# Performance work log

Hardware: AMD Instinct MI355X
Metric: run time of the kernel (lower is better)

The kernel has to match this reference:

```python
import jax, jax.numpy as jnp
import numpy as np

N_EXPERTS = 8
N_SHARED = 1
N_ROUTED = N_EXPERTS - N_SHARED          # 7
TOP_K_ROUTED = 3 - N_SHARED              # 2 routed experts per token
C = 1024
H = 4 * C


def _mlp(x, w_fc, w_proj):
    # x: [n, C]; w_fc: [C, H]; w_proj: [H, C]; exact (erf) GELU like torch nn.GELU
    return jax.nn.gelu(x @ w_fc, approximate=False) @ w_proj


def setup_inputs() -> dict:
    key = jax.random.key(0)
    ks = jax.random.split(key, 6)
    s = 0.02
    return {
        "x": jax.random.normal(ks[0], (4, 2048, C), dtype=jnp.float32),
        "gate_w": jax.random.normal(ks[1], (N_ROUTED, C), dtype=jnp.float32) * s,
        "lb_bias": jnp.zeros((N_ROUTED,), dtype=jnp.float32),
        "shared_wfc": jax.random.normal(ks[2], (C, H), dtype=jnp.float32) * s,
        "shared_wproj": jax.random.normal(ks[3], (H, C), dtype=jnp.float32) * s,
        "routed_wfc": jax.random.normal(ks[4], (N_ROUTED, C, H), dtype=jnp.float32) * s,
        "routed_wproj": jax.random.normal(ks[5], (N_ROUTED, H, C), dtype=jnp.float32) * s,
    }


def reference(x, gate_w, lb_bias, shared_wfc, shared_wproj, routed_wfc, routed_wproj):
    B, T, Cc = x.shape
    xt = x.reshape(-1, Cc)                       # [n, C]
    n = xt.shape[0]

    # shared expert(s) applied to every token
    shared_out = _mlp(xt, shared_wfc, shared_wproj)

    # routing
    routed_logits = xt @ gate_w.T                # [n, E_r]
    sel_logits = routed_logits + lb_bias
    _, topk_idx = jax.lax.top_k(sel_logits, TOP_K_ROUTED)   # [n, k]
    routed_probs = jax.nn.softmax(routed_logits.astype(jnp.float32), axis=-1)
    topk_w = jnp.take_along_axis(routed_probs, topk_idx, axis=-1)  # [n, k]

    # per-token combine weights over routed experts: [n, E_r]
    cw = jnp.zeros((n, N_ROUTED), dtype=jnp.float32)
    cw = cw.at[jnp.arange(n)[:, None], topk_idx].add(topk_w)

    # dispatch-combine: small fixed loop over routed experts
    routed_out = jnp.zeros_like(xt)
    for e in range(N_ROUTED):
        y = _mlp(xt, routed_wfc[e], routed_wproj[e])
        routed_out = routed_out + cw[:, e:e + 1] * y

    return (shared_out + routed_out).reshape(B, T, Cc)
```

## Files before the change

kernel.cpp:

```cpp
#include <hip/hip_runtime.h>
#include <hip/hip_bf16.h>

#define AS1 __attribute__((address_space(1)))
#define AS3 __attribute__((address_space(3)))

typedef __bf16 bf16x8 __attribute__((ext_vector_type(8)));
typedef float f32x4 __attribute__((ext_vector_type(4)));

static constexpr int C_DIM = 1024;
static constexpr int H_DIM = 4096;
static constexpr int NTOK  = 8192;
static constexpr int NR    = 7;
static constexpr int MAXG  = 17408;
static constexpr int MAXT  = 136;
static constexpr size_t WSZ = (size_t)C_DIM * H_DIM;

static __device__ __forceinline__ unsigned short f2bf(float f) {
  __hip_bfloat16 h = __float2bfloat16(f);
  return *reinterpret_cast<unsigned short*>(&h);
}

static __device__ __forceinline__ void gload16(const void* g, void* lds) {
  __builtin_amdgcn_global_load_lds((const AS1 void*)g, (AS3 void*)lds, 16, 0, 0);
}

__global__ __launch_bounds__(256) void cast_x_kernel(const float* __restrict__ x,
                                                     unsigned short* __restrict__ xb) {
  size_t i = ((size_t)blockIdx.x * blockDim.x + threadIdx.x) * 4;
  float4 v = *(const float4*)(x + i);
  ushort4 o;
  o.x = f2bf(v.x); o.y = f2bf(v.y); o.z = f2bf(v.z); o.w = f2bf(v.w);
  *(ushort4*)(xb + i) = o;
}

__global__ __launch_bounds__(256) void init_kernel(int* __restrict__ idx, int* __restrict__ cnt,
                                                   int* __restrict__ cursor) {
  int i = blockIdx.x * 256 + threadIdx.x;
  if (i < MAXG) idx[i] = 0;
  if (blockIdx.x == 0 && threadIdx.x < 8) { cnt[threadIdx.x] = 0; cursor[threadIdx.x] = 0; }
}

__global__ __launch_bounds__(256) void routing_kernel(const float* __restrict__ x,
                                                      const float* __restrict__ gw,
                                                      const float* __restrict__ bias,
                                                      float* __restrict__ cw,
                                                      int* __restrict__ cnt) {
  int wid = (int)((blockIdx.x * (size_t)blockDim.x + threadIdx.x) >> 6);
  int lane = threadIdx.x & 63;
  if (wid >= NTOK) return;
  const float* xt = x + (size_t)wid * C_DIM;
  float p[NR] = {0.f, 0.f, 0.f, 0.f, 0.f, 0.f, 0.f};
  for (int i = lane; i < C_DIM; i += 64) {
    float xv = xt[i];
#pragma unroll
    for (int e = 0; e < NR; ++e) p[e] += xv * gw[e * C_DIM + i];
  }
#pragma unroll
  for (int e = 0; e < NR; ++e) {
#pragma unroll
    for (int off = 32; off; off >>= 1) p[e] += __shfl_down(p[e], off);
  }
  if (lane == 0) {
    float m = p[0];
#pragma unroll
    for (int e = 1; e < NR; ++e) m = fmaxf(m, p[e]);
    float pr[NR], s = 0.f;
#pragma unroll
    for (int e = 0; e < NR; ++e) { pr[e] = __expf(p[e] - m); s += pr[e]; }
    float inv = 1.0f / s;
#pragma unroll
    for (int e = 0; e < NR; ++e) pr[e] *= inv;
    float sel[NR];
#pragma unroll
    for (int e = 0; e < NR; ++e) sel[e] = p[e] + bias[e];
    int i1 = 0;
#pragma unroll
    for (int e = 1; e < NR; ++e) if (sel[e] > sel[i1]) i1 = e;
    int i2 = -1;
#pragma unroll
    for (int e = 0; e < NR; ++e) {
      if (e == i1) continue;
      if (i2 < 0 || sel[e] > sel[i2]) i2 = e;
    }
    float c[NR] = {0.f, 0.f, 0.f, 0.f, 0.f, 0.f, 0.f};
    c[i1] = pr[i1];
    c[i2] += pr[i2];
#pragma unroll
    for (int e = 0; e < NR; ++e) cw[(size_t)wid * NR + e] = c[e];
    atomicAdd(&cnt[i1], 1);
    atomicAdd(&cnt[i2], 1);
  }
}

__global__ void scan_kernel(const int* __restrict__ cnt, int* __restrict__ offs,
                            int* __restrict__ tmap, int* __restrict__ ntiles) {
  int o = 0, nt = 0;
  for (int e = 0; e < NR; ++e) {
    offs[e] = o;
    int n = (cnt[e] + 127) & ~127;
    o += n;
    for (int tm = 0; tm < n; tm += 128) tmap[nt++] = (e << 16) | tm;
  }
  *ntiles = nt;
}

__global__ __launch_bounds__(256) void place_kernel(const float* __restrict__ cw,
                                                    const int* __restrict__ offs,
                                                    int* __restrict__ cursor,
                                                    int* __restrict__ idx,
                                                    int* __restrict__ tok2slot,
                                                    float* __restrict__ tok2w) {
  int t = blockIdx.x * 256 + threadIdx.x;
  if (t >= NTOK) return;
  int k = 0;
#pragma unroll
  for (int e = 0; e < NR; ++e) {
    float w = cw[(size_t)t * NR + e];
    if (w > 0.f) {
      int p = atomicAdd(&cursor[e], 1);
      int slot = offs[e] + p;
      idx[slot] = t;
      tok2slot[t * 2 + k] = slot;
      tok2w[t * 2 + k] = w;
      ++k;
    }
  }
}

__global__ void transpose_cast_all(const float* __restrict__ shared_w,
                                   const float* __restrict__ routed_w,
                                   unsigned short* __restrict__ out, int R, int S) {
  int e = blockIdx.z;
  const float* in = (e == 0) ? shared_w : routed_w + (size_t)(e - 1) * R * S;
  unsigned short* o = out + (size_t)e * R * S;
  __shared__ float t[32][33];
  int bx = blockIdx.x * 32;
  int by = blockIdx.y * 32;
  int tx = threadIdx.x, ty = threadIdx.y;
#pragma unroll
  for (int i = 0; i < 32; i += 8)
    t[ty + i][tx] = in[(size_t)(by + ty + i) * S + bx + tx];
  __syncthreads();
#pragma unroll
  for (int i = 0; i < 32; i += 8)
    o[(size_t)(bx + ty + i) * R + by + tx] = f2bf(t[tx][ty + i]);
}


template <bool GATHER>
__global__ __launch_bounds__(256) void gemm_fc(const unsigned short* __restrict__ A,
                                               const unsigned short* __restrict__ BtAll,
                                               unsigned short* __restrict__ Y,
                                               const int* __restrict__ idx,
                                               const int* __restrict__ offs,
                                               const int* __restrict__ tmap,
                                               const int* __restrict__ ntiles) {
  __shared__ __align__(16) unsigned short As[3][4096];
  __shared__ __align__(16) unsigned short Bs[3][4096];
  const int tid = threadIdx.x;
  const int wave = tid >> 6, lane = tid & 63;
  constexpr int NT = C_DIM / 32;

  int m0, n0, base;
  const unsigned short* Bt;
  if (GATHER) {
    if (blockIdx.y >= *ntiles) return;
    const int packed = tmap[blockIdx.y];
    const int e = packed >> 16;
    m0 = packed & 0xffff;
    n0 = blockIdx.x * 128;
    base = offs[e];
    Bt = BtAll + (size_t)(e + 1) * WSZ;
  } else {
    const int f = blockIdx.y * gridDim.x + blockIdx.x;
    const int cpx = (gridDim.x * gridDim.y) >> 3;
    const int swz = (f & 7) * cpx + (f >> 3);
    m0 = (swz / gridDim.x) * 128;
    n0 = (swz % gridDim.x) * 128;
    base = 0;
    Bt = BtAll;
  }

  const int q0 = wave * 128 + lane, q1 = q0 + 64;
  const int kg0 = q0 >> 7, r0 = q0 & 127;
  const int kg1 = q1 >> 7, r1 = q1 & 127;
  const size_t rowA0 = GATHER ? (size_t)idx[base + m0 + r0] : (size_t)(m0 + r0);
  const size_t rowA1 = GATHER ? (size_t)idx[base + m0 + r1] : (size_t)(m0 + r1);
  const unsigned short* gA0 = A + rowA0 * C_DIM + kg0 * 8;
  const unsigned short* gA1 = A + rowA1 * C_DIM + kg1 * 8;
  const unsigned short* gB0 = Bt + (size_t)(n0 + r0) * C_DIM + kg0 * 8;
  const unsigned short* gB1 = Bt + (size_t)(n0 + r1) * C_DIM + kg1 * 8;
  const int c0 = (wave * 2 + 0) * 512, c1 = (wave * 2 + 1) * 512;

  const int wr = wave >> 1, wc = wave & 1;
  const int fr = lane & 15, fq = lane >> 4;
  f32x4 acc[4][4] = {};

  asm volatile("s_waitcnt vmcnt(0)" ::: "memory");
  gload16(gA0, &As[0][c0]); gload16(gA1, &As[0][c1]);
  gload16(gB0, &Bs[0][c0]); gload16(gB1, &Bs[0][c1]);
  gload16(gA0 + 32, &As[1][c0]); gload16(gA1 + 32, &As[1][c1]);
  gload16(gB0 + 32, &Bs[1][c0]); gload16(gB1 + 32, &Bs[1][c1]);

  int rb = 0;
  for (int t = 0; t < NT; ++t) {
    if (t + 2 < NT) {
      const int wb = (rb >= 1) ? rb - 1 : rb + 2;
      const int nk = (t + 2) * 32;
      gload16(gA0 + nk, &As[wb][c0]); gload16(gA1 + nk, &As[wb][c1]);
      gload16(gB0 + nk, &Bs[wb][c0]); gload16(gB1 + nk, &Bs[wb][c1]);
      asm volatile("s_waitcnt vmcnt(8)" ::: "memory");
    } else if (t + 1 < NT) {
      asm volatile("s_waitcnt vmcnt(4)" ::: "memory");
    } else {
      asm volatile("s_waitcnt vmcnt(0)" ::: "memory");
    }
    __builtin_amdgcn_s_barrier();
    bf16x8 af[4], bfr[4];
#pragma unroll
    for (int m = 0; m < 4; ++m)
      af[m] = *(const bf16x8*)&As[rb][fq * 1024 + (wr * 64 + m * 16 + fr) * 8];
#pragma unroll
    for (int n = 0; n < 4; ++n)
      bfr[n] = *(const bf16x8*)&Bs[rb][fq * 1024 + (wc * 64 + n * 16 + fr) * 8];
#pragma unroll
    for (int m = 0; m < 4; ++m)
#pragma unroll
      for (int n = 0; n < 4; ++n)
        acc[m][n] = __builtin_amdgcn_mfma_f32_16x16x32_bf16(af[m], bfr[n], acc[m][n], 0, 0, 0);
    __builtin_amdgcn_s_barrier();
    rb = (rb == 2) ? 0 : rb + 1;
  }

#pragma unroll
  for (int m = 0; m < 4; ++m)
#pragma unroll
    for (int n = 0; n < 4; ++n)
#pragma unroll
      for (int j = 0; j < 4; ++j) {
        const int row = m0 + wr * 64 + m * 16 + fq * 4 + j;
        const int col = n0 + wc * 64 + n * 16 + fr;
        const float v = acc[m][n][j];
        const float g = 0.5f * v * (1.0f + erff(v * 0.70710678118654752f));
        Y[(size_t)(base + row) * H_DIM + col] = f2bf(g);
      }
}

template <bool ROUTED>
__global__ __launch_bounds__(256) void gemm_proj(const unsigned short* __restrict__ Yg,
                                                 const unsigned short* __restrict__ BtAll,
                                                 float* __restrict__ Out,
                                                 const int* __restrict__ offs,
                                                 const int* __restrict__ tmap,
                                                 const int* __restrict__ ntiles) {
  __shared__ __align__(16) unsigned short As[3][4096];
  __shared__ __align__(16) unsigned short Bs[3][4096];
  const int tid = threadIdx.x;
  const int wave = tid >> 6, lane = tid & 63;
  constexpr int NT = H_DIM / 32;

  int m0, n0, base;
  const unsigned short* Bt;
  if (ROUTED) {
    if (blockIdx.y >= *ntiles) return;
    const int packed = tmap[blockIdx.y];
    const int e = packed >> 16;
    m0 = packed & 0xffff;
    n0 = blockIdx.x * 128;
    base = offs[e];
    Bt = BtAll + (size_t)(e + 1) * WSZ;
  } else {
    const int f = blockIdx.y * gridDim.x + blockIdx.x;
    const int cpx = (gridDim.x * gridDim.y) >> 3;
    const int swz = (f & 7) * cpx + (f >> 3);
    m0 = (swz / gridDim.x) * 128;
    n0 = (swz % gridDim.x) * 128;
    base = 0;
    Bt = BtAll;
  }

  const int q0 = wave * 128 + lane, q1 = q0 + 64;
  const int kg0 = q0 >> 7, r0 = q0 & 127;
  const int kg1 = q1 >> 7, r1 = q1 & 127;
  const unsigned short* gA0 = Yg + (size_t)(base + m0 + r0) * H_DIM + kg0 * 8;
  const unsigned short* gA1 = Yg + (size_t)(base + m0 + r1) * H_DIM + kg1 * 8;
  const unsigned short* gB0 = Bt + (size_t)(n0 + r0) * H_DIM + kg0 * 8;
  const unsigned short* gB1 = Bt + (size_t)(n0 + r1) * H_DIM + kg1 * 8;
  const int c0 = (wave * 2 + 0) * 512, c1 = (wave * 2 + 1) * 512;

  const int wr = wave >> 1, wc = wave & 1;
  const int fr = lane & 15, fq = lane >> 4;
  f32x4 acc[4][4] = {};

  asm volatile("s_waitcnt vmcnt(0)" ::: "memory");
  gload16(gA0, &As[0][c0]); gload16(gA1, &As[0][c1]);
  gload16(gB0, &Bs[0][c0]); gload16(gB1, &Bs[0][c1]);
  gload16(gA0 + 32, &As[1][c0]); gload16(gA1 + 32, &As[1][c1]);
  gload16(gB0 + 32, &Bs[1][c0]); gload16(gB1 + 32, &Bs[1][c1]);

  int rb = 0;
  for (int t = 0; t < NT; ++t) {
    if (t + 2 < NT) {
      const int wb = (rb >= 1) ? rb - 1 : rb + 2;
      const int nk = (t + 2) * 32;
      gload16(gA0 + nk, &As[wb][c0]); gload16(gA1 + nk, &As[wb][c1]);
      gload16(gB0 + nk, &Bs[wb][c0]); gload16(gB1 + nk, &Bs[wb][c1]);
      asm volatile("s_waitcnt vmcnt(8)" ::: "memory");
    } else if (t + 1 < NT) {
      asm volatile("s_waitcnt vmcnt(4)" ::: "memory");
    } else {
      asm volatile("s_waitcnt vmcnt(0)" ::: "memory");
    }
    __builtin_amdgcn_s_barrier();
    bf16x8 af[4], bfr[4];
#pragma unroll
    for (int m = 0; m < 4; ++m)
      af[m] = *(const bf16x8*)&As[rb][fq * 1024 + (wr * 64 + m * 16 + fr) * 8];
#pragma unroll
    for (int n = 0; n < 4; ++n)
      bfr[n] = *(const bf16x8*)&Bs[rb][fq * 1024 + (wc * 64 + n * 16 + fr) * 8];
#pragma unroll
    for (int m = 0; m < 4; ++m)
#pragma unroll
      for (int n = 0; n < 4; ++n)
        acc[m][n] = __builtin_amdgcn_mfma_f32_16x16x32_bf16(af[m], bfr[n], acc[m][n], 0, 0, 0);
    __builtin_amdgcn_s_barrier();
    rb = (rb == 2) ? 0 : rb + 1;
  }

#pragma unroll
  for (int m = 0; m < 4; ++m)
#pragma unroll
    for (int n = 0; n < 4; ++n)
#pragma unroll
      for (int j = 0; j < 4; ++j) {
        const int p = wr * 64 + m * 16 + fq * 4 + j;
        const int col = n0 + wc * 64 + n * 16 + fr;
        const float v = acc[m][n][j];
        Out[(size_t)(base + m0 + p) * C_DIM + col] = v;
      }
}

__global__ __launch_bounds__(256) void combine_kernel(const float* __restrict__ Yout,
                                                      const int* __restrict__ tok2slot,
                                                      const float* __restrict__ tok2w,
                                                      float* __restrict__ out) {
  const int t = blockIdx.x;
  const int c4 = threadIdx.x;
  const int s0 = tok2slot[t * 2], s1 = tok2slot[t * 2 + 1];
  const float w0 = tok2w[t * 2], w1 = tok2w[t * 2 + 1];
  const float4 a = ((const float4*)(Yout + (size_t)s0 * C_DIM))[c4];
  const float4 b = ((const float4*)(Yout + (size_t)s1 * C_DIM))[c4];
  float4 o = ((float4*)(out + (size_t)t * C_DIM))[c4];
  o.x += w0 * a.x + w1 * b.x;
  o.y += w0 * a.y + w1 * b.y;
  o.z += w0 * a.z + w1 * b.z;
  o.w += w0 * a.w + w1 * b.w;
  ((float4*)(out + (size_t)t * C_DIM))[c4] = o;
}

extern "C" void kernel_launch(void* const* d_in, const int* in_sizes, int n_in,
                              void* d_out, int out_size, void* d_ws, size_t ws_size,
                              hipStream_t stream) {
  const float* x            = (const float*)d_in[0];
  const float* gate_w       = (const float*)d_in[1];
  const float* lb_bias      = (const float*)d_in[2];
  const float* shared_wfc   = (const float*)d_in[3];
  const float* shared_wproj = (const float*)d_in[4];
  const float* routed_wfc   = (const float*)d_in[5];
  const float* routed_wproj = (const float*)d_in[6];
  float* out = (float*)d_out;

  char* ws = (char*)d_ws;
  unsigned short* xb     = (unsigned short*)(ws);
  unsigned short* wfcT   = (unsigned short*)(ws + 16777216);
  float*          Yout   = (float*)(ws);
  unsigned short* wprojT = (unsigned short*)(ws + 83886080);
  unsigned short* Yg     = (unsigned short*)(ws + 150994944);
  float*          cw     = (float*)(ws + 293601280);
  int*            idx    = (int*)(ws + 293830656);
  int*            cnt    = (int*)(ws + 293900288);
  int*            offs   = (int*)(ws + 293900352);
  int*            cursor = (int*)(ws + 293900416);
  int*            tok2slot = (int*)(ws + 293900480);
  float*          tok2w    = (float*)(ws + 293966016);
  int*            tmap     = (int*)(ws + 294031552);
  int*            ntiles   = (int*)(ws + 294032128);

  cast_x_kernel<<<NTOK * C_DIM / (256 * 4), 256, 0, stream>>>(x, xb);
  init_kernel<<<(MAXG + 255) / 256, 256, 0, stream>>>(idx, cnt, cursor);
  routing_kernel<<<NTOK / 4, 256, 0, stream>>>(x, gate_w, lb_bias, cw, cnt);
  scan_kernel<<<1, 1, 0, stream>>>(cnt, offs, tmap, ntiles);
  place_kernel<<<NTOK / 256, 256, 0, stream>>>(cw, offs, cursor, idx, tok2slot, tok2w);

  transpose_cast_all<<<dim3(H_DIM / 32, C_DIM / 32, 8), dim3(32, 8), 0, stream>>>(
      shared_wfc, routed_wfc, wfcT, C_DIM, H_DIM);
  transpose_cast_all<<<dim3(C_DIM / 32, H_DIM / 32, 8), dim3(32, 8), 0, stream>>>(
      shared_wproj, routed_wproj, wprojT, H_DIM, C_DIM);

  gemm_fc<false><<<dim3(H_DIM / 128, NTOK / 128), 256, 0, stream>>>(
      xb, wfcT, Yg, idx, offs, tmap, ntiles);
  gemm_proj<false><<<dim3(C_DIM / 128, NTOK / 128), 256, 0, stream>>>(
      Yg, wprojT, out, offs, tmap, ntiles);

  gemm_fc<true><<<dim3(H_DIM / 128, MAXT), 256, 0, stream>>>(
      xb, wfcT, Yg, idx, offs, tmap, ntiles);
  gemm_proj<true><<<dim3(C_DIM / 128, MAXT), 256, 0, stream>>>(
      Yg, wprojT, Yout, offs, tmap, ntiles);

  combine_kernel<<<NTOK, 256, 0, stream>>>(Yout, tok2slot, tok2w, out);
}
```

Before: 1.282 ms.

## Merge fc/proj GEMMs into one 256x256-tile kernel with 512 threads

```diff
diff --git a/kernel.cpp b/kernel.cpp
--- a/kernel.cpp
+++ b/kernel.cpp
@@ -12,7 +12,8 @@
 static constexpr int NTOK  = 8192;
 static constexpr int NR    = 7;
 static constexpr int MAXG  = 17408;
-static constexpr int MAXT  = 136;
+static constexpr int MAXIDX = 17664;
+static constexpr int MAXT  = 72;
 static constexpr size_t WSZ = (size_t)C_DIM * H_DIM;
 
 static __device__ __forceinline__ unsigned short f2bf(float f) {
@@ -36,7 +37,7 @@
 __global__ __launch_bounds__(256) void init_kernel(int* __restrict__ idx, int* __restrict__ cnt,
                                                    int* __restrict__ cursor) {
   int i = blockIdx.x * 256 + threadIdx.x;
-  if (i < MAXG) idx[i] = 0;
+  if (i < MAXIDX) idx[i] = 0;
   if (blockIdx.x == 0 && threadIdx.x < 8) { cnt[threadIdx.x] = 0; cursor[threadIdx.x] = 0; }
 }
 
@@ -93,13 +94,18 @@
 }
 
 __global__ void scan_kernel(const int* __restrict__ cnt, int* __restrict__ offs,
-                            int* __restrict__ tmap, int* __restrict__ ntiles) {
+                            int* __restrict__ tmap, int* __restrict__ tlim,
+                            int* __restrict__ ntiles) {
   int o = 0, nt = 0;
   for (int e = 0; e < NR; ++e) {
     offs[e] = o;
-    int n = (cnt[e] + 127) & ~127;
-    o += n;
-    for (int tm = 0; tm < n; tm += 128) tmap[nt++] = (e << 16) | tm;
+    int a = (cnt[e] + 127) & ~127;
+    for (int tm = 0; tm < a; tm += 256) {
+      tmap[nt] = ((e + 1) << 20) | (o + tm);
+      tlim[nt] = o + a;
+      ++nt;
+    }
+    o += a;
   }
   *ntiles = nt;
 }
@@ -146,85 +152,89 @@
     o[(size_t)(bx + ty + i) * R + by + tx] = f2bf(t[tx][ty + i]);
 }
 
-
-template <bool GATHER>
-__global__ __launch_bounds__(256) void gemm_fc(const unsigned short* __restrict__ A,
-                                               const unsigned short* __restrict__ BtAll,
-                                               unsigned short* __restrict__ Y,
-                                               const int* __restrict__ idx,
-                                               const int* __restrict__ offs,
-                                               const int* __restrict__ tmap,
-                                               const int* __restrict__ ntiles) {
-  __shared__ __align__(16) unsigned short As[3][4096];
-  __shared__ __align__(16) unsigned short Bs[3][4096];
+template <int EPI, bool GATHER, int K>
+__global__ __launch_bounds__(512, 2) void gemm256(const unsigned short* __restrict__ A,
+                                                  const unsigned short* __restrict__ BtAll,
+                                                  unsigned short* __restrict__ Ybf,
+                                                  float* __restrict__ Out,
+                                                  const int* __restrict__ idx,
+                                                  const int* __restrict__ tmap,
+                                                  const int* __restrict__ tlim,
+                                                  const int* __restrict__ ntiles) {
+  __shared__ __align__(16) unsigned short As[3][8192];
+  __shared__ __align__(16) unsigned short Bs[3][8192];
+  constexpr int NT = K / 32;
   const int tid = threadIdx.x;
   const int wave = tid >> 6, lane = tid & 63;
-  constexpr int NT = C_DIM / 32;
-
-  int m0, n0, base;
+
+  const int b = blockIdx.y * gridDim.x + blockIdx.x;
+  const int tx = (b >> 3) % gridDim.x;
+  const int ty = (b & 7) + 8 * ((b >> 3) / gridDim.x);
+
+  int m0, lim;
   const unsigned short* Bt;
   if (GATHER) {
-    if (blockIdx.y >= *ntiles) return;
-    const int packed = tmap[blockIdx.y];
-    const int e = packed >> 16;
-    m0 = packed & 0xffff;
-    n0 = blockIdx.x * 128;
-    base = offs[e];
-    Bt = BtAll + (size_t)(e + 1) * WSZ;
+    if (ty >= *ntiles) return;
+    const int packed = tmap[ty];
+    m0 = packed & 0xfffff;
+    lim = tlim[ty];
+    Bt = BtAll + (size_t)(packed >> 20) * WSZ;
   } else {
-    const int f = blockIdx.y * gridDim.x + blockIdx.x;
-    const int cpx = (gridDim.x * gridDim.y) >> 3;
-    const int swz = (f & 7) * cpx + (f >> 3);
-    m0 = (swz / gridDim.x) * 128;
-    n0 = (swz % gridDim.x) * 128;
-    base = 0;
+    m0 = ty * 256;
+    lim = 1 << 30;
     Bt = BtAll;
   }
-
-  const int q0 = wave * 128 + lane, q1 = q0 + 64;
-  const int kg0 = q0 >> 7, r0 = q0 & 127;
-  const int kg1 = q1 >> 7, r1 = q1 & 127;
-  const size_t rowA0 = GATHER ? (size_t)idx[base + m0 + r0] : (size_t)(m0 + r0);
-  const size_t rowA1 = GATHER ? (size_t)idx[base + m0 + r1] : (size_t)(m0 + r1);
-  const unsigned short* gA0 = A + rowA0 * C_DIM + kg0 * 8;
-  const unsigned short* gA1 = A + rowA1 * C_DIM + kg1 * 8;
-  const unsigned short* gB0 = Bt + (size_t)(n0 + r0) * C_DIM + kg0 * 8;
-  const unsigned short* gB1 = Bt + (size_t)(n0 + r1) * C_DIM + kg1 * 8;
-  const int c0 = (wave * 2 + 0) * 512, c1 = (wave * 2 + 1) * 512;
-
-  const int wr = wave >> 1, wc = wave & 1;
+  const int n0 = tx * 256;
+
+  const int kg = tid >> 8;
+  const int r  = tid & 255;
+  int arow = m0 + r;
+  if (EPI == 0 && GATHER) arow = idx[arow];
+  const unsigned short* gA = A + (size_t)arow * K;
+  const unsigned short* gB = Bt + (size_t)(n0 + r) * K;
+  const int gA0off = kg * 8, gA1off = (kg + 2) * 8;
+  const int d0 = (wave >> 2) * 2048 + (wave & 3) * 512;
+  const int d1 = d0 + 4096;
+
+  const int wr = wave >> 2, wc = wave & 3;
   const int fr = lane & 15, fq = lane >> 4;
-  f32x4 acc[4][4] = {};
+  f32x4 acc[8][4] = {};
 
   asm volatile("s_waitcnt vmcnt(0)" ::: "memory");
-  gload16(gA0, &As[0][c0]); gload16(gA1, &As[0][c1]);
-  gload16(gB0, &Bs[0][c0]); gload16(gB1, &Bs[0][c1]);
-  gload16(gA0 + 32, &As[1][c0]); gload16(gA1 + 32, &As[1][c1]);
-  gload16(gB0 + 32, &Bs[1][c0]); gload16(gB1 + 32, &Bs[1][c1]);
+#pragma unroll
+  for (int t = 0; t < 2; ++t) {
+    const int nk = t * 32;
+    gload16(gA + nk + gA0off, &As[t][d0]);
+    gload16(gA + nk + gA1off, &As[t][d1]);
+    gload16(gB + nk + gA0off, &Bs[t][d0]);
+    gload16(gB + nk + gA1off, &Bs[t][d1]);
+  }
 
   int rb = 0;
   for (int t = 0; t < NT; ++t) {
-    if (t + 2 < NT) {
-      const int wb = (rb >= 1) ? rb - 1 : rb + 2;
-      const int nk = (t + 2) * 32;
-      gload16(gA0 + nk, &As[wb][c0]); gload16(gA1 + nk, &As[wb][c1]);
-      gload16(gB0 + nk, &Bs[wb][c0]); gload16(gB1 + nk, &Bs[wb][c1]);
-      asm volatile("s_waitcnt vmcnt(8)" ::: "memory");
-    } else if (t + 1 < NT) {
+    if (t + 1 < NT) {
       asm volatile("s_waitcnt vmcnt(4)" ::: "memory");
     } else {
       asm volatile("s_waitcnt vmcnt(0)" ::: "memory");
     }
     __builtin_amdgcn_s_barrier();
-    bf16x8 af[4], bfr[4];
-#pragma unroll
-    for (int m = 0; m < 4; ++m)
-      af[m] = *(const bf16x8*)&As[rb][fq * 1024 + (wr * 64 + m * 16 + fr) * 8];
+    if (t + 2 < NT) {
+      const int wb = (rb >= 1) ? rb - 1 : 2;
+      const int nk = (t + 2) * 32;
+      gload16(gA + nk + gA0off, &As[wb][d0]);
+      gload16(gA + nk + gA1off, &As[wb][d1]);
+      gload16(gB + nk + gA0off, &Bs[wb][d0]);
+      gload16(gB + nk + gA1off, &Bs[wb][d1]);
+    }
+    bf16x8 af[8], bfr[4];
+#pragma unroll
+    for (int m = 0; m < 8; ++m)
+      af[m] = *(const bf16x8*)&As[rb][fq * 2048 + (wr * 128 + m * 16 + fr) * 8];
 #pragma unroll
     for (int n = 0; n < 4; ++n)
-      bfr[n] = *(const bf16x8*)&Bs[rb][fq * 1024 + (wc * 64 + n * 16 + fr) * 8];
-#pragma unroll
-    for (int m = 0; m < 4; ++m)
+      bfr[n] = *(const bf16x8*)&Bs[rb][fq * 2048 + (wc * 64 + n * 16 + fr) * 8];
+#pragma unroll
+    for (int m = 0; m < 8; ++m)
 #pragma unroll
       for (int n = 0; n < 4; ++n)
         acc[m][n] = __builtin_amdgcn_mfma_f32_16x16x32_bf16(af[m], bfr[n], acc[m][n], 0, 0, 0);
@@ -233,111 +243,24 @@
   }
 
 #pragma unroll
-  for (int m = 0; m < 4; ++m)
+  for (int m = 0; m < 8; ++m)
 #pragma unroll
     for (int n = 0; n < 4; ++n)
 #pragma unroll
       for (int j = 0; j < 4; ++j) {
-        const int row = m0 + wr * 64 + m * 16 + fq * 4 + j;
+        const int slot = m0 + wr * 128 + m * 16 + fq * 4 + j;
         const int col = n0 + wc * 64 + n * 16 + fr;
         const float v = acc[m][n][j];
-        const float g = 0.5f * v * (1.0f + erff(v * 0.70710678118654752f));
-        Y[(size_t)(base + row) * H_DIM + col] = f2bf(g);
-      }
-}
-
-template <bool ROUTED>
-__global__ __launch_bounds__(256) void gemm_proj(const unsigned short* __restrict__ Yg,
-                                                 const unsigned short* __restrict__ BtAll,
-                                                 float* __restrict__ Out,
-                                                 const int* __restrict__ offs,
-                                                 const int* __restrict__ tmap,
-                                                 const int* __restrict__ ntiles) {
-  __shared__ __align__(16) unsigned short As[3][4096];
-  __shared__ __align__(16) unsigned short Bs[3][4096];
-  const int tid = threadIdx.x;
-  const int wave = tid >> 6, lane = tid & 63;
-  constexpr int NT = H_DIM / 32;
-
-  int m0, n0, base;
-  const unsigned short* Bt;
-  if (ROUTED) {
-    if (blockIdx.y >= *ntiles) return;
-    const int packed = tmap[blockIdx.y];
-    const int e = packed >> 16;
-    m0 = packed & 0xffff;
-    n0 = blockIdx.x * 128;
-    base = offs[e];
-    Bt = BtAll + (size_t)(e + 1) * WSZ;
-  } else {
-    const int f = blockIdx.y * gridDim.x + blockIdx.x;
-    const int cpx = (gridDim.x * gridDim.y) >> 3;
-    const int swz = (f & 7) * cpx + (f >> 3);
-    m0 = (swz / gridDim.x) * 128;
-    n0 = (swz % gridDim.x) * 128;
-    base = 0;
-    Bt = BtAll;
-  }
-
-  const int q0 = wave * 128 + lane, q1 = q0 + 64;
-  const int kg0 = q0 >> 7, r0 = q0 & 127;
-  const int kg1 = q1 >> 7, r1 = q1 & 127;
-  const unsigned short* gA0 = Yg + (size_t)(base + m0 + r0) * H_DIM + kg0 * 8;
-  const unsigned short* gA1 = Yg + (size_t)(base + m0 + r1) * H_DIM + kg1 * 8;
-  const unsigned short* gB0 = Bt + (size_t)(n0 + r0) * H_DIM + kg0 * 8;
-  const unsigned short* gB1 = Bt + (size_t)(n0 + r1) * H_DIM + kg1 * 8;
-  const int c0 = (wave * 2 + 0) * 512, c1 = (wave * 2 + 1) * 512;
-
-  const int wr = wave >> 1, wc = wave & 1;
-  const int fr = lane & 15, fq = lane >> 4;
-  f32x4 acc[4][4] = {};
-
-  asm volatile("s_waitcnt vmcnt(0)" ::: "memory");
-  gload16(gA0, &As[0][c0]); gload16(gA1, &As[0][c1]);
-  gload16(gB0, &Bs[0][c0]); gload16(gB1, &Bs[0][c1]);
-  gload16(gA0 + 32, &As[1][c0]); gload16(gA1 + 32, &As[1][c1]);
-  gload16(gB0 + 32, &Bs[1][c0]); gload16(gB1 + 32, &Bs[1][c1]);
-
-  int rb = 0;
-  for (int t = 0; t < NT; ++t) {
-    if (t + 2 < NT) {
-      const int wb = (rb >= 1) ? rb - 1 : rb + 2;
-      const int nk = (t + 2) * 32;
-      gload16(gA0 + nk, &As[wb][c0]); gload16(gA1 + nk, &As[wb][c1]);
-      gload16(gB0 + nk, &Bs[wb][c0]); gload16(gB1 + nk, &Bs[wb][c1]);
-      asm volatile("s_waitcnt vmcnt(8)" ::: "memory");
-    } else if (t + 1 < NT) {
-      asm volatile("s_waitcnt vmcnt(4)" ::: "memory");
-    } else {
-      asm volatile("s_waitcnt vmcnt(0)" ::: "memory");
-    }
-    __builtin_amdgcn_s_barrier();
-    bf16x8 af[4], bfr[4];
-#pragma unroll
-    for (int m = 0; m < 4; ++m)
-      af[m] = *(const bf16x8*)&As[rb][fq * 1024 + (wr * 64 + m * 16 + fr) * 8];
-#pragma unroll
-    for (int n = 0; n < 4; ++n)
-      bfr[n] = *(const bf16x8*)&Bs[rb][fq * 1024 + (wc * 64 + n * 16 + fr) * 8];
-#pragma unroll
-    for (int m = 0; m < 4; ++m)
-#pragma unroll
-      for (int n = 0; n < 4; ++n)
-        acc[m][n] = __builtin_amdgcn_mfma_f32_16x16x32_bf16(af[m], bfr[n], acc[m][n], 0, 0, 0);
-    __builtin_amdgcn_s_barrier();
-    rb = (rb == 2) ? 0 : rb + 1;
-  }
-
-#pragma unroll
-  for (int m = 0; m < 4; ++m)
-#pragma unroll
-    for (int n = 0; n < 4; ++n)
-#pragma unroll
-      for (int j = 0; j < 4; ++j) {
-        const int p = wr * 64 + m * 16 + fq * 4 + j;
-        const int col = n0 + wc * 64 + n * 16 + fr;
-        const float v = acc[m][n][j];
-        Out[(size_t)(base + m0 + p) * C_DIM + col] = v;
+        if (EPI == 0) {
+          if (!GATHER || slot < lim) {
+            const float g = 0.5f * v * (1.0f + erff(v * 0.70710678118654752f));
+            Ybf[(size_t)slot * H_DIM + col] = f2bf(g);
+          }
+        } else if (EPI == 1) {
+          Out[(size_t)slot * C_DIM + col] = v;
+        } else {
+          if (slot < lim) Out[(size_t)slot * C_DIM + col] = v;
+        }
       }
 }
 
@@ -379,18 +302,19 @@
   unsigned short* Yg     = (unsigned short*)(ws + 150994944);
   float*          cw     = (float*)(ws + 293601280);
   int*            idx    = (int*)(ws + 293830656);
-  int*            cnt    = (int*)(ws + 293900288);
-  int*            offs   = (int*)(ws + 293900352);
-  int*            cursor = (int*)(ws + 293900416);
-  int*            tok2slot = (int*)(ws + 293900480);
-  float*          tok2w    = (float*)(ws + 293966016);
-  int*            tmap     = (int*)(ws + 294031552);
-  int*            ntiles   = (int*)(ws + 294032128);
+  int*            cnt    = (int*)(ws + 293901312);
+  int*            offs   = (int*)(ws + 293901376);
+  int*            cursor = (int*)(ws + 293901440);
+  int*            tok2slot = (int*)(ws + 293901504);
+  float*          tok2w    = (float*)(ws + 293967040);
+  int*            tmap     = (int*)(ws + 294032576);
+  int*            tlim     = (int*)(ws + 294032864);
+  int*            ntiles   = (int*)(ws + 294033152);
 
   cast_x_kernel<<<NTOK * C_DIM / (256 * 4), 256, 0, stream>>>(x, xb);
-  init_kernel<<<(MAXG + 255) / 256, 256, 0, stream>>>(idx, cnt, cursor);
+  init_kernel<<<(MAXIDX + 255) / 256, 256, 0, stream>>>(idx, cnt, cursor);
   routing_kernel<<<NTOK / 4, 256, 0, stream>>>(x, gate_w, lb_bias, cw, cnt);
-  scan_kernel<<<1, 1, 0, stream>>>(cnt, offs, tmap, ntiles);
+  scan_kernel<<<1, 1, 0, stream>>>(cnt, offs, tmap, tlim, ntiles);
   place_kernel<<<NTOK / 256, 256, 0, stream>>>(cw, offs, cursor, idx, tok2slot, tok2w);
 
   transpose_cast_all<<<dim3(H_DIM / 32, C_DIM / 32, 8), dim3(32, 8), 0, stream>>>(
@@ -398,15 +322,15 @@
   transpose_cast_all<<<dim3(C_DIM / 32, H_DIM / 32, 8), dim3(32, 8), 0, stream>>>(
       shared_wproj, routed_wproj, wprojT, H_DIM, C_DIM);
 
-  gemm_fc<false><<<dim3(H_DIM / 128, NTOK / 128), 256, 0, stream>>>(
-      xb, wfcT, Yg, idx, offs, tmap, ntiles);
-  gemm_proj<false><<<dim3(C_DIM / 128, NTOK / 128), 256, 0, stream>>>(
-      Yg, wprojT, out, offs, tmap, ntiles);
-
-  gemm_fc<true><<<dim3(H_DIM / 128, MAXT), 256, 0, stream>>>(
-      xb, wfcT, Yg, idx, offs, tmap, ntiles);
-  gemm_proj<true><<<dim3(C_DIM / 128, MAXT), 256, 0, stream>>>(
-      Yg, wprojT, Yout, offs, tmap, ntiles);
+  gemm256<0, false, C_DIM><<<dim3(H_DIM / 256, NTOK / 256), 512, 0, stream>>>(
+      xb, wfcT, Yg, nullptr, idx, tmap, tlim, ntiles);
+  gemm256<1, false, H_DIM><<<dim3(C_DIM / 256, NTOK / 256), 512, 0, stream>>>(
+      Yg, wprojT, nullptr, out, idx, tmap, tlim, ntiles);
+
+  gemm256<0, true, C_DIM><<<dim3(H_DIM / 256, MAXT), 512, 0, stream>>>(
+      xb, wfcT, Yg, nullptr, idx, tmap, tlim, ntiles);
+  gemm256<2, true, H_DIM><<<dim3(C_DIM / 256, MAXT), 512, 0, stream>>>(
+      Yg, wprojT, nullptr, Yout, idx, tmap, tlim, ntiles);
 
   combine_kernel<<<NTOK, 256, 0, stream>>>(Yout, tok2slot, tok2w, out);
 }
```

After: 1.541 ms. 1.2x slower.

## Split-K routed projection GEMM with bf16 partials, swizzle routed fc tiles

Applied to the files above, without the earlier changes.

```diff
diff --git a/kernel.cpp b/kernel.cpp
--- a/kernel.cpp
+++ b/kernel.cpp
@@ -11,13 +11,17 @@
 static constexpr int H_DIM = 4096;
 static constexpr int NTOK  = 8192;
 static constexpr int NR    = 7;
-static constexpr int MAXG  = 17408;
+static constexpr int NSLOT = 17408;
 static constexpr int MAXT  = 136;
 static constexpr size_t WSZ = (size_t)C_DIM * H_DIM;
 
 static __device__ __forceinline__ unsigned short f2bf(float f) {
   __hip_bfloat16 h = __float2bfloat16(f);
   return *reinterpret_cast<unsigned short*>(&h);
+}
+static __device__ __forceinline__ float bf2f(unsigned short u) {
+  unsigned int v = ((unsigned int)u) << 16;
+  return *reinterpret_cast<float*>(&v);
 }
 
 static __device__ __forceinline__ void gload16(const void* g, void* lds) {
@@ -36,7 +40,7 @@
 __global__ __launch_bounds__(256) void init_kernel(int* __restrict__ idx, int* __restrict__ cnt,
                                                    int* __restrict__ cursor) {
   int i = blockIdx.x * 256 + threadIdx.x;
-  if (i < MAXG) idx[i] = 0;
+  if (i < NSLOT) idx[i] = 0;
   if (blockIdx.x == 0 && threadIdx.x < 8) { cnt[threadIdx.x] = 0; cursor[threadIdx.x] = 0; }
 }
 
@@ -161,22 +165,24 @@
   const int wave = tid >> 6, lane = tid & 63;
   constexpr int NT = C_DIM / 32;
 
+  const int f = blockIdx.y * gridDim.x + blockIdx.x;
+  const int cpx = (gridDim.x * gridDim.y) >> 3;
+  const int swz = (f & 7) * cpx + (f >> 3);
+  const int bx = swz % gridDim.x, ty = swz / gridDim.x;
+
   int m0, n0, base;
   const unsigned short* Bt;
   if (GATHER) {
-    if (blockIdx.y >= *ntiles) return;
-    const int packed = tmap[blockIdx.y];
+    if (ty >= *ntiles) return;
+    const int packed = tmap[ty];
     const int e = packed >> 16;
     m0 = packed & 0xffff;
-    n0 = blockIdx.x * 128;
+    n0 = bx * 128;
     base = offs[e];
     Bt = BtAll + (size_t)(e + 1) * WSZ;
   } else {
-    const int f = blockIdx.y * gridDim.x + blockIdx.x;
-    const int cpx = (gridDim.x * gridDim.y) >> 3;
-    const int swz = (f & 7) * cpx + (f >> 3);
-    m0 = (swz / gridDim.x) * 128;
-    n0 = (swz % gridDim.x) * 128;
+    m0 = ty * 128;
+    n0 = bx * 128;
     base = 0;
     Bt = BtAll;
   }
@@ -205,7 +211,7 @@
   int rb = 0;
   for (int t = 0; t < NT; ++t) {
     if (t + 2 < NT) {
-      const int wb = (rb >= 1) ? rb - 1 : rb + 2;
+      const int wb = (rb >= 1) ? rb - 1 : 2;
       const int nk = (t + 2) * 32;
       gload16(gA0 + nk, &As[wb][c0]); gload16(gA1 + nk, &As[wb][c1]);
       gload16(gB0 + nk, &Bs[wb][c0]); gload16(gB1 + nk, &Bs[wb][c1]);
@@ -246,44 +252,26 @@
       }
 }
 
-template <bool ROUTED>
-__global__ __launch_bounds__(256) void gemm_proj(const unsigned short* __restrict__ Yg,
-                                                 const unsigned short* __restrict__ BtAll,
-                                                 float* __restrict__ Out,
-                                                 const int* __restrict__ offs,
-                                                 const int* __restrict__ tmap,
-                                                 const int* __restrict__ ntiles) {
+__global__ __launch_bounds__(256) void gemm_proj_shared(const unsigned short* __restrict__ Yg,
+                                                        const unsigned short* __restrict__ Bt,
+                                                        float* __restrict__ Out) {
   __shared__ __align__(16) unsigned short As[3][4096];
   __shared__ __align__(16) unsigned short Bs[3][4096];
   const int tid = threadIdx.x;
   const int wave = tid >> 6, lane = tid & 63;
   constexpr int NT = H_DIM / 32;
 
-  int m0, n0, base;
-  const unsigned short* Bt;
-  if (ROUTED) {
-    if (blockIdx.y >= *ntiles) return;
-    const int packed = tmap[blockIdx.y];
-    const int e = packed >> 16;
-    m0 = packed & 0xffff;
-    n0 = blockIdx.x * 128;
-    base = offs[e];
-    Bt = BtAll + (size_t)(e + 1) * WSZ;
-  } else {
-    const int f = blockIdx.y * gridDim.x + blockIdx.x;
-    const int cpx = (gridDim.x * gridDim.y) >> 3;
-    const int swz = (f & 7) * cpx + (f >> 3);
-    m0 = (swz / gridDim.x) * 128;
-    n0 = (swz % gridDim.x) * 128;
-    base = 0;
-    Bt = BtAll;
-  }
+  const int f = blockIdx.y * gridDim.x + blockIdx.x;
+  const int cpx = (gridDim.x * gridDim.y) >> 3;
+  const int swz = (f & 7) * cpx + (f >> 3);
+  const int m0 = (swz / gridDim.x) * 128;
+  const int n0 = (swz % gridDim.x) * 128;
 
   const int q0 = wave * 128 + lane, q1 = q0 + 64;
   const int kg0 = q0 >> 7, r0 = q0 & 127;
   const int kg1 = q1 >> 7, r1 = q1 & 127;
-  const unsigned short* gA0 = Yg + (size_t)(base + m0 + r0) * H_DIM + kg0 * 8;
-  const unsigned short* gA1 = Yg + (size_t)(base + m0 + r1) * H_DIM + kg1 * 8;
+  const unsigned short* gA0 = Yg + (size_t)(m0 + r0) * H_DIM + kg0 * 8;
+  const unsigned short* gA1 = Yg + (size_t)(m0 + r1) * H_DIM + kg1 * 8;
   const unsigned short* gB0 = Bt + (size_t)(n0 + r0) * H_DIM + kg0 * 8;
   const unsigned short* gB1 = Bt + (size_t)(n0 + r1) * H_DIM + kg1 * 8;
   const int c0 = (wave * 2 + 0) * 512, c1 = (wave * 2 + 1) * 512;
@@ -292,7 +280,6 @@
   const int fr = lane & 15, fq = lane >> 4;
   f32x4 acc[4][4] = {};
 
-  asm volatile("s_waitcnt vmcnt(0)" ::: "memory");
   gload16(gA0, &As[0][c0]); gload16(gA1, &As[0][c1]);
   gload16(gB0, &Bs[0][c0]); gload16(gB1, &Bs[0][c1]);
   gload16(gA0 + 32, &As[1][c0]); gload16(gA1 + 32, &As[1][c1]);
@@ -301,7 +288,7 @@
   int rb = 0;
   for (int t = 0; t < NT; ++t) {
     if (t + 2 < NT) {
-      const int wb = (rb >= 1) ? rb - 1 : rb + 2;
+      const int wb = (rb >= 1) ? rb - 1 : 2;
       const int nk = (t + 2) * 32;
       gload16(gA0 + nk, &As[wb][c0]); gload16(gA1 + nk, &As[wb][c1]);
       gload16(gB0 + nk, &Bs[wb][c0]); gload16(gB1 + nk, &Bs[wb][c1]);
@@ -336,27 +323,115 @@
       for (int j = 0; j < 4; ++j) {
         const int p = wr * 64 + m * 16 + fq * 4 + j;
         const int col = n0 + wc * 64 + n * 16 + fr;
-        const float v = acc[m][n][j];
-        Out[(size_t)(base + m0 + p) * C_DIM + col] = v;
+        Out[(size_t)(m0 + p) * C_DIM + col] = acc[m][n][j];
       }
 }
 
-__global__ __launch_bounds__(256) void combine_kernel(const float* __restrict__ Yout,
+__global__ __launch_bounds__(256) void gemm_proj_routed(const unsigned short* __restrict__ Yg,
+                                                        const unsigned short* __restrict__ BtAll,
+                                                        unsigned short* __restrict__ Pb,
+                                                        const int* __restrict__ offs,
+                                                        const int* __restrict__ tmap,
+                                                        const int* __restrict__ ntiles) {
+  __shared__ __align__(16) unsigned short As[3][4096];
+  __shared__ __align__(16) unsigned short Bs[3][4096];
+  const int tid = threadIdx.x;
+  const int wave = tid >> 6, lane = tid & 63;
+  constexpr int KSEG = H_DIM / 2;
+  constexpr int NT = KSEG / 32;
+  const int kbase = blockIdx.z * KSEG;
+
+  const int f = blockIdx.y * gridDim.x + blockIdx.x;
+  const int cpx = (gridDim.x * gridDim.y) >> 3;
+  const int swz = (f & 7) * cpx + (f >> 3);
+  const int bx = swz % gridDim.x, ty = swz / gridDim.x;
+
+  if (ty >= *ntiles) return;
+  const int packed = tmap[ty];
+  const int e = packed >> 16;
+  const int m0 = packed & 0xffff;
+  const int n0 = bx * 128;
+  const int base = offs[e];
+  const unsigned short* Bt = BtAll + (size_t)(e + 1) * WSZ;
+
+  const int q0 = wave * 128 + lane, q1 = q0 + 64;
+  const int kg0 = q0 >> 7, r0 = q0 & 127;
+  const int kg1 = q1 >> 7, r1 = q1 & 127;
+  const unsigned short* gA0 = Yg + (size_t)(base + m0 + r0) * H_DIM + kbase + kg0 * 8;
+  const unsigned short* gA1 = Yg + (size_t)(base + m0 + r1) * H_DIM + kbase + kg1 * 8;
+  const unsigned short* gB0 = Bt + (size_t)(n0 + r0) * H_DIM + kbase + kg0 * 8;
+  const unsigned short* gB1 = Bt + (size_t)(n0 + r1) * H_DIM + kbase + kg1 * 8;
+  const int c0 = (wave * 2 + 0) * 512, c1 = (wave * 2 + 1) * 512;
+
+  const int wr = wave >> 1, wc = wave & 1;
+  const int fr = lane & 15, fq = lane >> 4;
+  f32x4 acc[4][4] = {};
+
+  gload16(gA0, &As[0][c0]); gload16(gA1, &As[0][c1]);
+  gload16(gB0, &Bs[0][c0]); gload16(gB1, &Bs[0][c1]);
+  gload16(gA0 + 32, &As[1][c0]); gload16(gA1 + 32, &As[1][c1]);
+  gload16(gB0 + 32, &Bs[1][c0]); gload16(gB1 + 32, &Bs[1][c1]);
+
+  int rb = 0;
+  for (int t = 0; t < NT; ++t) {
+    if (t + 2 < NT) {
+      const int wb = (rb >= 1) ? rb - 1 : 2;
+      const int nk = (t + 2) * 32;
+      gload16(gA0 + nk, &As[wb][c0]); gload16(gA1 + nk, &As[wb][c1]);
+      gload16(gB0 + nk, &Bs[wb][c0]); gload16(gB1 + nk, &Bs[wb][c1]);
+      asm volatile("s_waitcnt vmcnt(8)" ::: "memory");
+    } else if (t + 1 < NT) {
+      asm volatile("s_waitcnt vmcnt(4)" ::: "memory");
+    } else {
+      asm volatile("s_waitcnt vmcnt(0)" ::: "memory");
+    }
+    __builtin_amdgcn_s_barrier();
+    bf16x8 af[4], bfr[4];
+#pragma unroll
+    for (int m = 0; m < 4; ++m)
+      af[m] = *(const bf16x8*)&As[rb][fq * 1024 + (wr * 64 + m * 16 + fr) * 8];
+#pragma unroll
+    for (int n = 0; n < 4; ++n)
+      bfr[n] = *(const bf16x8*)&Bs[rb][fq * 1024 + (wc * 64 + n * 16 + fr) * 8];
+#pragma unroll
+    for (int m = 0; m < 4; ++m)
+#pragma unroll
+      for (int n = 0; n < 4; ++n)
+        acc[m][n] = __builtin_amdgcn_mfma_f32_16x16x32_bf16(af[m], bfr[n], acc[m][n], 0, 0, 0);
+    __builtin_amdgcn_s_barrier();
+    rb = (rb == 2) ? 0 : rb + 1;
+  }
+
+#pragma unroll
+  for (int m = 0; m < 4; ++m)
+#pragma unroll
+    for (int n = 0; n < 4; ++n)
+#pragma unroll
+      for (int j = 0; j < 4; ++j) {
+        const int p = wr * 64 + m * 16 + fq * 4 + j;
+        const int col = n0 + wc * 64 + n * 16 + fr;
+        Pb[((size_t)blockIdx.z * NSLOT + base + m0 + p) * C_DIM + col] = f2bf(acc[m][n][j]);
+      }
+}
+
+__global__ __launch_bounds__(256) void combine_kernel(const unsigned short* __restrict__ P,
                                                       const int* __restrict__ tok2slot,
                                                       const float* __restrict__ tok2w,
                                                       float* __restrict__ out) {
   const int t = blockIdx.x;
-  const int c4 = threadIdx.x;
+  const int c = threadIdx.x * 4;
   const int s0 = tok2slot[t * 2], s1 = tok2slot[t * 2 + 1];
   const float w0 = tok2w[t * 2], w1 = tok2w[t * 2 + 1];
-  const float4 a = ((const float4*)(Yout + (size_t)s0 * C_DIM))[c4];
-  const float4 b = ((const float4*)(Yout + (size_t)s1 * C_DIM))[c4];
-  float4 o = ((float4*)(out + (size_t)t * C_DIM))[c4];
-  o.x += w0 * a.x + w1 * b.x;
-  o.y += w0 * a.y + w1 * b.y;
-  o.z += w0 * a.z + w1 * b.z;
-  o.w += w0 * a.w + w1 * b.w;
-  ((float4*)(out + (size_t)t * C_DIM))[c4] = o;
+  const ushort4 a0 = *(const ushort4*)&P[((size_t)0 * NSLOT + s0) * C_DIM + c];
+  const ushort4 a1 = *(const ushort4*)&P[((size_t)1 * NSLOT + s0) * C_DIM + c];
+  const ushort4 b0 = *(const ushort4*)&P[((size_t)0 * NSLOT + s1) * C_DIM + c];
+  const ushort4 b1 = *(const ushort4*)&P[((size_t)1 * NSLOT + s1) * C_DIM + c];
+  float4 o = *(float4*)&out[(size_t)t * C_DIM + c];
+  o.x += w0 * (bf2f(a0.x) + bf2f(a1.x)) + w1 * (bf2f(b0.x) + bf2f(b1.x));
+  o.y += w0 * (bf2f(a0.y) + bf2f(a1.y)) + w1 * (bf2f(b0.y) + bf2f(b1.y));
+  o.z += w0 * (bf2f(a0.z) + bf2f(a1.z)) + w1 * (bf2f(b0.z) + bf2f(b1.z));
+  o.w += w0 * (bf2f(a0.w) + bf2f(a1.w)) + w1 * (bf2f(b0.w) + bf2f(b1.w));
+  *(float4*)&out[(size_t)t * C_DIM + c] = o;
 }
 
 extern "C" void kernel_launch(void* const* d_in, const int* in_sizes, int n_in,
@@ -374,21 +449,21 @@
   char* ws = (char*)d_ws;
   unsigned short* xb     = (unsigned short*)(ws);
   unsigned short* wfcT   = (unsigned short*)(ws + 16777216);
-  float*          Yout   = (float*)(ws);
+  unsigned short* Pb     = (unsigned short*)(ws);
   unsigned short* wprojT = (unsigned short*)(ws + 83886080);
   unsigned short* Yg     = (unsigned short*)(ws + 150994944);
   float*          cw     = (float*)(ws + 293601280);
   int*            idx    = (int*)(ws + 293830656);
-  int*            cnt    = (int*)(ws + 293900288);
-  int*            offs   = (int*)(ws + 293900352);
-  int*            cursor = (int*)(ws + 293900416);
-  int*            tok2slot = (int*)(ws + 293900480);
-  float*          tok2w    = (float*)(ws + 293966016);
-  int*            tmap     = (int*)(ws + 294031552);
-  int*            ntiles   = (int*)(ws + 294032128);
+  int*            cnt    = (int*)(ws + 293901312);
+  int*            offs   = (int*)(ws + 293901376);
+  int*            cursor = (int*)(ws + 293901440);
+  int*            tok2slot = (int*)(ws + 293901504);
+  float*          tok2w    = (float*)(ws + 293967040);
+  int*            tmap     = (int*)(ws + 294032576);
+  int*            ntiles   = (int*)(ws + 294033152);
 
   cast_x_kernel<<<NTOK * C_DIM / (256 * 4), 256, 0, stream>>>(x, xb);
-  init_kernel<<<(MAXG + 255) / 256, 256, 0, stream>>>(idx, cnt, cursor);
+  init_kernel<<<(NSLOT + 255) / 256, 256, 0, stream>>>(idx, cnt, cursor);
   routing_kernel<<<NTOK / 4, 256, 0, stream>>>(x, gate_w, lb_bias, cw, cnt);
   scan_kernel<<<1, 1, 0, stream>>>(cnt, offs, tmap, ntiles);
   place_kernel<<<NTOK / 256, 256, 0, stream>>>(cw, offs, cursor, idx, tok2slot, tok2w);
@@ -400,13 +475,12 @@
 
   gemm_fc<false><<<dim3(H_DIM / 128, NTOK / 128), 256, 0, stream>>>(
       xb, wfcT, Yg, idx, offs, tmap, ntiles);
-  gemm_proj<false><<<dim3(C_DIM / 128, NTOK / 128), 256, 0, stream>>>(
-      Yg, wprojT, out, offs, tmap, ntiles);
+  gemm_proj_shared<<<dim3(C_DIM / 128, NTOK / 128), 256, 0, stream>>>(Yg, wprojT, out);
 
   gemm_fc<true><<<dim3(H_DIM / 128, MAXT), 256, 0, stream>>>(
       xb, wfcT, Yg, idx, offs, tmap, ntiles);
-  gemm_proj<true><<<dim3(C_DIM / 128, MAXT), 256, 0, stream>>>(
-      Yg, wprojT, Yout, offs, tmap, ntiles);
-
-  combine_kernel<<<NTOK, 256, 0, stream>>>(Yout, tok2slot, tok2w, out);
-}
+  gemm_proj_routed<<<dim3(C_DIM / 128, MAXT, 2), 256, 0, stream>>>(
+      Yg, wprojT, Pb, offs, tmap, ntiles);
+
+  combine_kernel<<<NTOK, 256, 0, stream>>>(Pb, tok2slot, tok2w, out);
+}
```

After: 1.238 ms. 3.5% less time.
